# Performance work log

Hardware: AMD Instinct MI355X
Metric: run time of the kernel (lower is better)

The kernel has to match this reference:

```python
import jax, jax.numpy as jnp
import numpy as np


def _dct_basis(N):
    # X[k] = 2 * sum_n x[n] * cos(pi * k * (2n+1) / (2N))  -- matches the
    # flip+concat+rfft+twiddle path of the torch module (unnormalized DCT-II x2).
    k = jnp.arange(N, dtype=jnp.float32)[:, None]
    n = jnp.arange(N, dtype=jnp.float32)[None, :]
    return 2.0 * jnp.cos(jnp.pi * k * (2.0 * n + 1.0) / (2.0 * N))  # (K, N)


def _dct2(x):
    B, C, H, W = x.shape
    Bw = _dct_basis(W)
    Bh = _dct_basis(H)
    x = jnp.einsum('bchw,kw->bchk', x, Bw)  # DCT along W
    x = jnp.einsum('bchw,kh->bckw', x, Bh)  # DCT along H
    return x


def _conv3x3(x, w, b):
    y = jax.lax.conv_general_dilated(x, w, window_strides=(1, 1), padding='SAME',
                                     dimension_numbers=('NCHW', 'OIHW', 'NCHW'))
    return y + b[None, :, None, None]


def _bn(x, g, be, m, v):
    # inference-mode BatchNorm2d, eps = 1e-5
    inv = jax.lax.rsqrt(v + 1e-5)
    return (x - m[None, :, None, None]) * (g * inv)[None, :, None, None] + be[None, :, None, None]


def setup_inputs() -> dict:
    key = jax.random.key(0)
    ks = jax.random.split(key, 16)
    B, C, H, W = 32, 1, 224, 224
    mid, emb = 128, 256
    s = 0.05
    return {
        'x':  jax.random.normal(ks[0], (B, C, H, W), jnp.float32),
        'w1': jax.random.normal(ks[1], (64, C, 3, 3), jnp.float32) * s,
        'b1': jax.random.normal(ks[2], (64,), jnp.float32) * s,
        'g1': jax.random.uniform(ks[3], (64,), jnp.float32, 0.5, 1.5),
        'be1': jax.random.normal(ks[4], (64,), jnp.float32) * s,
        'm1': jax.random.normal(ks[5], (64,), jnp.float32) * s,
        'v1': jax.random.uniform(ks[6], (64,), jnp.float32, 0.5, 1.5),
        'w2': jax.random.normal(ks[7], (mid, 64, 3, 3), jnp.float32) * s,
        'b2': jax.random.normal(ks[8], (mid,), jnp.float32) * s,
        'g2': jax.random.uniform(ks[9], (mid,), jnp.float32, 0.5, 1.5),
        'be2': jax.random.normal(ks[10], (mid,), jnp.float32) * s,
        'm2': jax.random.normal(ks[11], (mid,), jnp.float32) * s,
        'v2': jax.random.uniform(ks[12], (mid,), jnp.float32, 0.5, 1.5),
        'wp': jax.random.normal(ks[13], (emb, mid), jnp.float32) * s,
        'bp': jax.random.normal(ks[14], (emb,), jnp.float32) * s,
    }


def reference(x, w1, b1, g1, be1, m1, v1, w2, b2, g2, be2, m2, v2, wp, bp):
    USE_TOPK = 0.5
    X = _dct2(x)                                   # (B, 1, H, W)
    B, C, H, W = X.shape
    k_h, k_w = int(H * USE_TOPK), int(W * USE_TOPK)
    mask = jnp.zeros((H, W), X.dtype).at[:k_h, :k_w].set(1.0)
    X = X * mask[None, None]
    h = jax.nn.relu(_bn(_conv3x3(X, w1, b1), g1, be1, m1, v1))
    h = jax.nn.relu(_bn(_conv3x3(h, w2, b2), g2, be2, m2, v2))
    h = jnp.mean(h, axis=(2, 3))                   # AdaptiveAvgPool2d((1,1)) -> (B, mid)
    return h @ wp.T + bp                           # (B, emb_dim)
```

## Files before the change

kernel.cpp:

```cpp
#include <hip/hip_runtime.h>
#include <math.h>


#define NPIX 224
#define KEEP 112
#define H1DIM 115
#define NPX1 (H1DIM * H1DIM)
#define ADIM 114

typedef short bf16x8 __attribute__((ext_vector_type(8)));
typedef float f32x4  __attribute__((ext_vector_type(4)));
typedef float f32x16 __attribute__((ext_vector_type(16)));

__device__ __forceinline__ unsigned short f2bf(float f) {
    unsigned int u = __float_as_uint(f);
    unsigned int r = (u + 0x7FFFu + ((u >> 16) & 1u)) >> 16;
    return (unsigned short)r;
}

__global__ __launch_bounds__(256) void prep_kernel(
    const float* __restrict__ w1, const float* __restrict__ b1,
    const float* __restrict__ g1, const float* __restrict__ be1,
    const float* __restrict__ m1, const float* __restrict__ v1,
    const float* __restrict__ w2,
    float* __restrict__ Bst, float* __restrict__ P,
    float* __restrict__ ws1, float* __restrict__ wb1,
    uint4* __restrict__ w2f) {
    int bx = blockIdx.x, tid = threadIdx.x;
    if (bx < 49) {
        int idx = bx * 256 + tid;
        if (idx < KEEP * KEEP) {
            int n = idx / KEEP, k = idx - n * KEEP;
            double ang = 3.14159265358979323846 * (double)k * (2.0 * n + 1.0) / (2.0 * NPIX);
            Bst[n * KEEP + k] = (float)(2.0 * cos(ang));
        }
    } else if (bx < 54) {
        __shared__ float c1s[64];
        if (tid < 64) {
            float sc = g1[tid] * rsqrtf(v1[tid] + 1e-5f);
            c1s[tid] = fmaxf((b1[tid] - m1[tid]) * sc + be1[tid], 0.f);
        }
        __syncthreads();
        int idx = (bx - 49) * 256 + tid;
        if (idx < 128 * 9) {
            int oc = idx / 9, tap = idx - oc * 9;
            float s = 0.f;
            for (int ic = 0; ic < 64; ++ic)
                s = fmaf(w2[((size_t)oc * 64 + ic) * 9 + tap], c1s[ic], s);
            P[idx] = s;
        }
    } else if (bx == 54) {
        if (tid < 64) {
            float sc = g1[tid] * rsqrtf(v1[tid] + 1e-5f);
            wb1[tid] = (b1[tid] - m1[tid]) * sc + be1[tid];
            for (int t = 0; t < 9; ++t) ws1[tid * 9 + t] = w1[tid * 9 + t] * sc;
        }
    } else {
        int j = (bx - 55) * 256 + tid;
        if (j < 9216) {
            int q = j >> 6, lane = j & 63;
            int tap = q / 16, rem = q & 15;
            int kc = rem >> 2, g32 = rem & 3;
            int oc = g32 * 32 + (lane & 31);
            int ic0 = kc * 16 + (lane >> 5) * 8;
            union { unsigned short us[8]; uint4 v; } u;
#pragma unroll
            for (int t_ = 0; t_ < 8; ++t_)
                u.us[t_] = f2bf(w2[((size_t)oc * 64 + ic0 + t_) * 9 + tap]);
            w2f[j] = u.v;
        }
    }
}

__global__ __launch_bounds__(128) void dct_w_kernel(const float* __restrict__ x,
                                                    const float* __restrict__ Bst,
                                                    float* __restrict__ tmp1) {
    int blk = blockIdx.x;
    int tid = threadIdx.x;
    __shared__ float eo[2][4][112];
    const float* rows = x + (size_t)blk * 4 * NPIX;
    for (int i = tid; i < 448; i += 128) {
        int r = i / 112, n = i - r * 112;
        float a = rows[r * NPIX + n], bv = rows[r * NPIX + 223 - n];
        eo[0][r][n] = a + bv;
        eo[1][r][n] = a - bv;
    }
    __syncthreads();
    int kw = tid;
    if (kw >= KEEP) return;
    const float* eop = &eo[kw & 1][0][0];
    float a0 = 0.f, a1 = 0.f, a2 = 0.f, a3 = 0.f;
    for (int n = 0; n < 112; ++n) {
        float bs = Bst[n * KEEP + kw];
        a0 = fmaf(eop[n], bs, a0);
        a1 = fmaf(eop[112 + n], bs, a1);
        a2 = fmaf(eop[224 + n], bs, a2);
        a3 = fmaf(eop[336 + n], bs, a3);
    }
    size_t base = (size_t)blk * 4 * KEEP + kw;
    tmp1[base] = a0; tmp1[base + 112] = a1; tmp1[base + 224] = a2; tmp1[base + 336] = a3;
}

__global__ __launch_bounds__(512) void dct_h_kernel(const float* __restrict__ tmp1,
                                                    const float* __restrict__ Bst,
                                                    float* __restrict__ Xd) {
    int kq = blockIdx.x, b = blockIdx.y;
    int tid = threadIdx.x;
    int kw = tid & 127, sub = tid >> 7;
    __shared__ float ps[3][4][112];
    const int kh0 = kq * 4;
    float a0 = 0.f, a1 = 0.f, a2 = 0.f, a3 = 0.f;
    if (kw < KEEP) {
        const float* t = tmp1 + (size_t)b * NPIX * KEEP + kw;
        for (int h = sub * 28; h < sub * 28 + 28; ++h) {
            float lo = t[(size_t)h * KEEP];
            float hi = t[(size_t)(223 - h) * KEEP];
            float e = lo + hi, o = lo - hi;
            const float* bs = Bst + h * KEEP + kh0;
            a0 = fmaf(e, bs[0], a0);
            a1 = fmaf(o, bs[1], a1);
            a2 = fmaf(e, bs[2], a2);
            a3 = fmaf(o, bs[3], a3);
        }
        if (sub) {
            ps[sub - 1][0][kw] = a0; ps[sub - 1][1][kw] = a1;
            ps[sub - 1][2][kw] = a2; ps[sub - 1][3][kw] = a3;
        }
    }
    __syncthreads();
    if (sub == 0 && kw < KEEP) {
        a0 += ps[0][0][kw] + ps[1][0][kw] + ps[2][0][kw];
        a1 += ps[0][1][kw] + ps[1][1][kw] + ps[2][1][kw];
        a2 += ps[0][2][kw] + ps[1][2][kw] + ps[2][2][kw];
        a3 += ps[0][3][kw] + ps[1][3][kw] + ps[2][3][kw];
        float* X = Xd + ((size_t)b * KEEP + kh0) * KEEP + kw;
        X[0] = a0; X[112] = a1; X[224] = a2; X[336] = a3;
    }
}

__global__ __launch_bounds__(256) void conv1_kernel(const float* __restrict__ Xd,
                                                    const float* __restrict__ ws1,
                                                    const float* __restrict__ wb1,
                                                    unsigned short* __restrict__ h1c) {
    const int b = blockIdx.y;
    const int p0 = blockIdx.x * 256;
    const int tid = threadIdx.x;
    const int p = p0 + tid;
    __shared__ uint4 Lt[2048];

    const bool valid = p < NPX1;
    int r = p / H1DIM, c = p - r * H1DIM;
    const float* X = Xd + (size_t)b * KEEP * KEEP;
    float xv[9];
#pragma unroll
    for (int ky = 0; ky < 3; ++ky)
#pragma unroll
        for (int kx = 0; kx < 3; ++kx) {
            int rr = r + ky - 1, cc = c + kx - 1;
            xv[ky * 3 + kx] =
                (valid && (unsigned)rr < (unsigned)KEEP && (unsigned)cc < (unsigned)KEEP)
                    ? X[rr * KEEP + cc] : 0.f;
        }

#pragma unroll 1
    for (int icg = 0; icg < 8; ++icg) {
        union { unsigned short us[8]; uint4 v; } u;
#pragma unroll
        for (int j = 0; j < 8; ++j) {
            int ic = icg * 8 + j;
            float s = wb1[ic];
#pragma unroll
            for (int t = 0; t < 9; ++t) s = fmaf(xv[t], ws1[ic * 9 + t], s);
            u.us[j] = f2bf(fmaxf(s, 0.f));
        }
        Lt[tid * 8 + (icg ^ (tid & 7))] = u.v;
    }
    __syncthreads();

#pragma unroll
    for (int k = 0; k < 8; ++k) {
        int q = k * 256 + tid;
        int pxl = q >> 3, ig = q & 7;
        uint4 v = Lt[pxl * 8 + (ig ^ (pxl & 7))];
        int pg = p0 + pxl;
        if (pg < NPX1)
            *reinterpret_cast<uint4*>(h1c + ((size_t)b * NPX1 + pg) * 64 + ig * 8) = v;
    }
}

__global__ __launch_bounds__(512, 4) void conv2_mfma_kernel(
    const unsigned short* __restrict__ h1c, const uint4* __restrict__ w2f,
    const float* __restrict__ b2, const float* __restrict__ g2,
    const float* __restrict__ be2, const float* __restrict__ m2,
    const float* __restrict__ v2, float* __restrict__ partial) {
    const int tc = blockIdx.x, tr = blockIdx.y, b = blockIdx.z;
    const int r0 = tr * 16, c0 = tc * 16;
    const int tid = threadIdx.x;
    const int lane = tid & 63, w = tid >> 6;
    const int mg = w & 3, og = w >> 2;

    __shared__ unsigned short At[324 * 64];

    const unsigned short* __restrict__ h1b = h1c + (size_t)b * (NPX1 * 64);
    char* Atw = reinterpret_cast<char*>(At);
    for (int e = tid; e < 2592; e += 512) {
        int px = e >> 3, gi = e & 7;
        int pr = px / 18, pc = px - pr * 18;
        int gr = r0 + pr - 1, gc = c0 + pc - 1;
        uint4 v = make_uint4(0u, 0u, 0u, 0u);
        if ((unsigned)gr < (unsigned)H1DIM && (unsigned)gc < (unsigned)H1DIM)
            v = *reinterpret_cast<const uint4*>(h1b + ((size_t)(gr * H1DIM + gc)) * 64 + gi * 8);
        int off = px * 128 + 32 * ((gi >> 1) ^ (px & 3)) + 16 * ((gi & 1) ^ ((px >> 2) & 1));
        *reinterpret_cast<uint4*>(Atw + off) = v;
    }
    __syncthreads();

    f32x16 acc[2][2];
#pragma unroll
    for (int F = 0; F < 2; ++F)
#pragma unroll
        for (int N = 0; N < 2; ++N)
#pragma unroll
            for (int i = 0; i < 16; ++i) acc[F][N][i] = 0.f;

    const int flim2 = ADIM - r0 - 4 * mg;
    int A0[9];
    {
        const int prb = 4 * mg + ((lane & 31) >> 4);
        const int cb = lane & 15;
        const int hb = lane >> 5;
#pragma unroll
        for (int ky = 0; ky < 3; ++ky)
#pragma unroll
            for (int kx = 0; kx < 3; ++kx) {
                int px = (prb + ky) * 18 + cb + kx;
                A0[ky * 3 + kx] = px * 128 + 32 * (px & 3) + 16 * (hb ^ ((px >> 2) & 1));
            }
    }
    const char* Atc = reinterpret_cast<const char*>(At);

    if (flim2 >= 4) {
#pragma unroll
        for (int s = 0; s < 36; ++s) {
            const int tap = s >> 2, kc = s & 3;
            const int ky = tap / 3, kx = tap - 3 * ky;
            const bf16x8* bq = reinterpret_cast<const bf16x8*>(
                w2f + (size_t)(((tap * 4 + kc) * 4) + og * 2) * 64 + lane);
            const bf16x8 b0 = bq[0];
            const bf16x8 b1 = bq[64];
            const int a0 = A0[ky * 3 + kx] ^ (kc << 5);
            const int a1 = (a0 ^ 16) + 4608;
            const bf16x8 va0 = *reinterpret_cast<const bf16x8*>(Atc + a0);
            const bf16x8 va1 = *reinterpret_cast<const bf16x8*>(Atc + a1);
            acc[0][0] = __builtin_amdgcn_mfma_f32_32x32x16_bf16(va0, b0, acc[0][0], 0, 0, 0);
            acc[0][1] = __builtin_amdgcn_mfma_f32_32x32x16_bf16(va0, b1, acc[0][1], 0, 0, 0);
            acc[1][0] = __builtin_amdgcn_mfma_f32_32x32x16_bf16(va1, b0, acc[1][0], 0, 0, 0);
            acc[1][1] = __builtin_amdgcn_mfma_f32_32x32x16_bf16(va1, b1, acc[1][1], 0, 0, 0);
        }
    } else if (flim2 > 0) {
#pragma unroll
        for (int s = 0; s < 36; ++s) {
            const int tap = s >> 2, kc = s & 3;
            const int ky = tap / 3, kx = tap - 3 * ky;
            const bf16x8* bq = reinterpret_cast<const bf16x8*>(
                w2f + (size_t)(((tap * 4 + kc) * 4) + og * 2) * 64 + lane);
            const bf16x8 b0 = bq[0];
            const bf16x8 b1 = bq[64];
            const int a0 = A0[ky * 3 + kx] ^ (kc << 5);
            const bf16x8 va0 = *reinterpret_cast<const bf16x8*>(Atc + a0);
            acc[0][0] = __builtin_amdgcn_mfma_f32_32x32x16_bf16(va0, b0, acc[0][0], 0, 0, 0);
            acc[0][1] = __builtin_amdgcn_mfma_f32_32x32x16_bf16(va0, b1, acc[0][1], 0, 0, 0);
        }
    }

    const int tile = tr * 8 + tc;
    float* pslice = partial + (((size_t)b * 64 + tile) * 4 + mg) * 128;
#pragma unroll
    for (int N = 0; N < 2; ++N) {
        int oc = og * 64 + N * 32 + (lane & 31);
        float sc = g2[oc] * rsqrtf(v2[oc] + 1e-5f);
        float bias = b2[oc] - m2[oc];
        float add = be2[oc];
        float s = 0.f;
#pragma unroll
        for (int F = 0; F < 2; ++F) {
#pragma unroll
            for (int rg = 0; rg < 16; ++rg) {
                int m = (rg & 3) + 8 * (rg >> 2) + 4 * (lane >> 5);
                int p = ((2 * mg + F) << 5) + m;
                int row = r0 + (p >> 4);
                int col = c0 + (p & 15);
                float v = fmaxf(fmaf(acc[F][N][rg] + bias, sc, add), 0.f);
                s += (row < ADIM && col < ADIM) ? v : 0.f;
            }
        }
        s += __shfl_xor(s, 32);
        if (lane < 32) pslice[og * 64 + N * 32 + lane] = s;
    }
}

__global__ __launch_bounds__(256) void reduce_mean_kernel(
    const float* __restrict__ partial, const float* __restrict__ P,
    const float* __restrict__ b2, const float* __restrict__ g2,
    const float* __restrict__ be2, const float* __restrict__ m2,
    const float* __restrict__ v2, float* __restrict__ mean) {
    int b = blockIdx.x, ocg = blockIdx.y;
    int tid = threadIdx.x;
    int ocl = tid & 15, jq = tid >> 4;
    int oc = ocg * 16 + ocl;
    const float* pb = partial + (size_t)b * 256 * 128 + oc;
    float s = 0.f;
#pragma unroll
    for (int jj = 0; jj < 16; ++jj) s += pb[(size_t)(jq * 16 + jj) * 128];
    __shared__ float red[16][17];
    red[jq][ocl] = s;
    __syncthreads();
    if (jq == 0) {
        float tot = 0.f;
#pragma unroll
        for (int k = 0; k < 16; ++k) tot += red[k][ocl];

        float p[9];
#pragma unroll
        for (int t = 0; t < 9; ++t) p[t] = P[oc * 9 + t];

        float Sall = p[0] + p[1] + p[2] + p[3] + p[4] + p[5] + p[6] + p[7] + p[8];
        float Stop = p[3] + p[4] + p[5] + p[6] + p[7] + p[8];
        float Sbot = p[0] + p[1] + p[2] + p[3] + p[4] + p[5];
        float Sleft  = p[1] + p[2] + p[4] + p[5] + p[7] + p[8];
        float Sright = p[0] + p[1] + p[3] + p[4] + p[6] + p[7];
        float Ctr = p[3] + p[4] + p[6] + p[7];
        float Cbl = p[1] + p[2] + p[4] + p[5];
        float Cbr = p[0] + p[1] + p[3] + p[4];

        float bias = b2[oc], mm = m2[oc], bb = be2[oc];
        float sc = g2[oc] * rsqrtf(v2[oc] + 1e-5f);
#define VALOF(S) fmaxf(((bias) + (S) - (mm)) * (sc) + (bb), 0.f)
        float cs = 36515.f * VALOF(Sall) + 109.f * VALOF(Stop) + 109.f * VALOF(Sleft)
                 + 222.f * VALOF(Sbot) + 222.f * VALOF(Sright)
                 + VALOF(Ctr) + VALOF(Cbl) + VALOF(Cbr);
#undef VALOF
        mean[b * 128 + oc] = (tot + cs) * (1.f / (224.f * 224.f));
    }
}

__global__ __launch_bounds__(256) void final_linear_kernel(const float* __restrict__ mean,
                                                           const float* __restrict__ wp,
                                                           const float* __restrict__ bp,
                                                           float* __restrict__ out) {
    int b = blockIdx.x, e = threadIdx.x;
    __shared__ float mrow[128];
    if (threadIdx.x < 128) mrow[threadIdx.x] = mean[b * 128 + threadIdx.x];
    __syncthreads();
    const float4* wr = reinterpret_cast<const float4*>(wp + (size_t)e * 128);
    float s = bp[e];
#pragma unroll 8
    for (int c = 0; c < 32; ++c) {
        float4 wv = wr[c];
        s = fmaf(mrow[4 * c], wv.x, s);
        s = fmaf(mrow[4 * c + 1], wv.y, s);
        s = fmaf(mrow[4 * c + 2], wv.z, s);
        s = fmaf(mrow[4 * c + 3], wv.w, s);
    }
    out[(size_t)b * 256 + e] = s;
}

extern "C" void kernel_launch(void* const* d_in, const int* in_sizes, int n_in,
                              void* d_out, int out_size, void* d_ws, size_t ws_size,
                              hipStream_t stream) {
    const float* x   = (const float*)d_in[0];
    const float* w1  = (const float*)d_in[1];
    const float* b1  = (const float*)d_in[2];
    const float* g1  = (const float*)d_in[3];
    const float* be1 = (const float*)d_in[4];
    const float* m1  = (const float*)d_in[5];
    const float* v1  = (const float*)d_in[6];
    const float* w2  = (const float*)d_in[7];
    const float* b2  = (const float*)d_in[8];
    const float* g2  = (const float*)d_in[9];
    const float* be2 = (const float*)d_in[10];
    const float* m2  = (const float*)d_in[11];
    const float* v2  = (const float*)d_in[12];
    const float* wp  = (const float*)d_in[13];
    const float* bp  = (const float*)d_in[14];
    float* out = (float*)d_out;

    float* ws = (float*)d_ws;
    size_t off = 0;
    float* Bst  = ws + off; off += (size_t)KEEP * KEEP;
    float* tmp1 = ws + off; off += (size_t)32 * NPIX * KEEP;
    float* Xd   = ws + off; off += (size_t)32 * KEEP * KEEP;
    float* P    = ws + off; off += 128 * 9;
    float* ws1  = ws + off; off += 64 * 9;
    float* wb1  = ws + off; off += 64;
    uint4* w2f  = (uint4*)(ws + off); off += (size_t)9216 * 4;
    float* part = ws + off; off += (size_t)32 * 256 * 128;
    float* mean = ws + off; off += 32 * 128;
    unsigned short* h1c = (unsigned short*)(ws + off);
    off += (size_t)32 * NPX1 * 64 / 2;

    if (ws_size < off * sizeof(float)) return;

    prep_kernel<<<dim3(91), dim3(256), 0, stream>>>(w1, b1, g1, be1, m1, v1, w2,
                                                    Bst, P, ws1, wb1, w2f);
    dct_w_kernel<<<dim3(32 * 56), dim3(128), 0, stream>>>(x, Bst, tmp1);
    dct_h_kernel<<<dim3(28, 32), dim3(512), 0, stream>>>(tmp1, Bst, Xd);
    conv1_kernel<<<dim3(52, 32), dim3(256), 0, stream>>>(Xd, ws1, wb1, h1c);
    conv2_mfma_kernel<<<dim3(8, 8, 32), dim3(512), 0, stream>>>(
        h1c, w2f, b2, g2, be2, m2, v2, part);
    reduce_mean_kernel<<<dim3(32, 8), dim3(256), 0, stream>>>(part, P, b2, g2, be2, m2, v2, mean);
    final_linear_kernel<<<dim3(32), dim3(256), 0, stream>>>(mean, wp, bp, out);
}
```

Measured before the change: 125.1 us.

## Enlarge conv2 tiles with split-channel staging, fuse reduce and linear tail

The conv2 MFMA kernel now covers 32x16 output tiles per block, with four row fragments per wave. It stages the input halo in two 32-channel halves through a smaller shared buffer, so each weight fragment feeds more MFMAs and far fewer blocks are launched. The reduce-mean and final linear kernels are merged into one tail kernel, and the DCT-W kernel now handles 8 rows per block with 256 threads. The cost is more accumulator registers (occupancy hint lowered to 2), an extra barrier per channel half, and per-fragment predicates in the inner loop.

```diff
diff --git a/kernel.cpp b/kernel.cpp
--- a/kernel.cpp
+++ b/kernel.cpp
@@ -9,7 +9,6 @@
 #define ADIM 114
 
 typedef short bf16x8 __attribute__((ext_vector_type(8)));
-typedef float f32x4  __attribute__((ext_vector_type(4)));
 typedef float f32x16 __attribute__((ext_vector_type(16)));
 
 __device__ __forceinline__ unsigned short f2bf(float f) {
@@ -26,22 +25,22 @@
     float* __restrict__ Bst, float* __restrict__ P,
     float* __restrict__ ws1, float* __restrict__ wb1,
     uint4* __restrict__ w2f) {
-    int bx = blockIdx.x, tid = threadIdx.x;
-    if (bx < 49) {
-        int idx = bx * 256 + tid;
+    int bp = blockIdx.x, tid = threadIdx.x;
+    if (bp < 49) {
+        int idx = bp * 256 + tid;
         if (idx < KEEP * KEEP) {
             int n = idx / KEEP, k = idx - n * KEEP;
             double ang = 3.14159265358979323846 * (double)k * (2.0 * n + 1.0) / (2.0 * NPIX);
             Bst[n * KEEP + k] = (float)(2.0 * cos(ang));
         }
-    } else if (bx < 54) {
+    } else if (bp < 54) {
         __shared__ float c1s[64];
         if (tid < 64) {
             float sc = g1[tid] * rsqrtf(v1[tid] + 1e-5f);
             c1s[tid] = fmaxf((b1[tid] - m1[tid]) * sc + be1[tid], 0.f);
         }
         __syncthreads();
-        int idx = (bx - 49) * 256 + tid;
+        int idx = (bp - 49) * 256 + tid;
         if (idx < 128 * 9) {
             int oc = idx / 9, tap = idx - oc * 9;
             float s = 0.f;
@@ -49,20 +48,20 @@
                 s = fmaf(w2[((size_t)oc * 64 + ic) * 9 + tap], c1s[ic], s);
             P[idx] = s;
         }
-    } else if (bx == 54) {
+    } else if (bp == 54) {
         if (tid < 64) {
             float sc = g1[tid] * rsqrtf(v1[tid] + 1e-5f);
             wb1[tid] = (b1[tid] - m1[tid]) * sc + be1[tid];
             for (int t = 0; t < 9; ++t) ws1[tid * 9 + t] = w1[tid * 9 + t] * sc;
         }
     } else {
-        int j = (bx - 55) * 256 + tid;
+        int j = (bp - 55) * 256 + tid;
         if (j < 9216) {
             int q = j >> 6, lane = j & 63;
             int tap = q / 16, rem = q & 15;
-            int kc = rem >> 2, g32 = rem & 3;
+            int kcq = rem >> 2, g32 = rem & 3;
             int oc = g32 * 32 + (lane & 31);
-            int ic0 = kc * 16 + (lane >> 5) * 8;
+            int ic0 = kcq * 16 + (lane >> 5) * 8;
             union { unsigned short us[8]; uint4 v; } u;
 #pragma unroll
             for (int t_ = 0; t_ < 8; ++t_)
@@ -72,23 +71,22 @@
     }
 }
 
-__global__ __launch_bounds__(128) void dct_w_kernel(const float* __restrict__ x,
+__global__ __launch_bounds__(256) void dct_w_kernel(const float* __restrict__ x,
                                                     const float* __restrict__ Bst,
                                                     float* __restrict__ tmp1) {
-    int blk = blockIdx.x;
-    int tid = threadIdx.x;
-    __shared__ float eo[2][4][112];
-    const float* rows = x + (size_t)blk * 4 * NPIX;
-    for (int i = tid; i < 448; i += 128) {
+    int bx = blockIdx.x, tid = threadIdx.x;
+    __shared__ float eo[2][8][112];
+    const float* rows = x + (size_t)bx * 8 * NPIX;
+    for (int i = tid; i < 896; i += 256) {
         int r = i / 112, n = i - r * 112;
         float a = rows[r * NPIX + n], bv = rows[r * NPIX + 223 - n];
         eo[0][r][n] = a + bv;
         eo[1][r][n] = a - bv;
     }
     __syncthreads();
-    int kw = tid;
+    int kw = tid & 127, rh = tid >> 7;
     if (kw >= KEEP) return;
-    const float* eop = &eo[kw & 1][0][0];
+    const float* eop = &eo[kw & 1][rh * 4][0];
     float a0 = 0.f, a1 = 0.f, a2 = 0.f, a3 = 0.f;
     for (int n = 0; n < 112; ++n) {
         float bs = Bst[n * KEEP + kw];
@@ -97,7 +95,7 @@
         a2 = fmaf(eop[224 + n], bs, a2);
         a3 = fmaf(eop[336 + n], bs, a3);
     }
-    size_t base = (size_t)blk * 4 * KEEP + kw;
+    size_t base = ((size_t)bx * 8 + rh * 4) * KEEP + kw;
     tmp1[base] = a0; tmp1[base + 112] = a1; tmp1[base + 224] = a2; tmp1[base + 336] = a3;
 }
 
@@ -188,142 +186,143 @@
     }
 }
 
-__global__ __launch_bounds__(512, 4) void conv2_mfma_kernel(
+__global__ __launch_bounds__(512, 2) void conv2_mfma_kernel(
     const unsigned short* __restrict__ h1c, const uint4* __restrict__ w2f,
     const float* __restrict__ b2, const float* __restrict__ g2,
     const float* __restrict__ be2, const float* __restrict__ m2,
     const float* __restrict__ v2, float* __restrict__ partial) {
     const int tc = blockIdx.x, tr = blockIdx.y, b = blockIdx.z;
-    const int r0 = tr * 16, c0 = tc * 16;
+    const int r0 = tr * 32, c0 = tc * 16;
     const int tid = threadIdx.x;
     const int lane = tid & 63, w = tid >> 6;
-    const int mg = w & 3, og = w >> 2;
-
-    __shared__ unsigned short At[324 * 64];
-
-    const unsigned short* __restrict__ h1b = h1c + (size_t)b * (NPX1 * 64);
-    char* Atw = reinterpret_cast<char*>(At);
-    for (int e = tid; e < 2592; e += 512) {
-        int px = e >> 3, gi = e & 7;
-        int pr = px / 18, pc = px - pr * 18;
-        int gr = r0 + pr - 1, gc = c0 + pc - 1;
-        uint4 v = make_uint4(0u, 0u, 0u, 0u);
-        if ((unsigned)gr < (unsigned)H1DIM && (unsigned)gc < (unsigned)H1DIM)
-            v = *reinterpret_cast<const uint4*>(h1b + ((size_t)(gr * H1DIM + gc)) * 64 + gi * 8);
-        int off = px * 128 + 32 * ((gi >> 1) ^ (px & 3)) + 16 * ((gi & 1) ^ ((px >> 2) & 1));
-        *reinterpret_cast<uint4*>(Atw + off) = v;
-    }
-    __syncthreads();
-
-    f32x16 acc[2][2];
-#pragma unroll
-    for (int F = 0; F < 2; ++F)
+    const int mgr = w & 3, ogr = w >> 2;
+
+    __shared__ uint4 AtV[2448];
+    char* Atw = reinterpret_cast<char*>(AtV);
+    const char* Atc = reinterpret_cast<const char*>(AtV);
+
+    f32x16 acc[4][2];
+#pragma unroll
+    for (int F = 0; F < 4; ++F)
 #pragma unroll
         for (int N = 0; N < 2; ++N)
 #pragma unroll
             for (int i = 0; i < 16; ++i) acc[F][N][i] = 0.f;
 
-    const int flim2 = ADIM - r0 - 4 * mg;
     int A0[9];
     {
-        const int prb = 4 * mg + ((lane & 31) >> 4);
+        const int rb = 2 * mgr + ((lane & 31) >> 4);
         const int cb = lane & 15;
         const int hb = lane >> 5;
 #pragma unroll
         for (int ky = 0; ky < 3; ++ky)
 #pragma unroll
             for (int kx = 0; kx < 3; ++kx) {
-                int px = (prb + ky) * 18 + cb + kx;
-                A0[ky * 3 + kx] = px * 128 + 32 * (px & 3) + 16 * (hb ^ ((px >> 2) & 1));
+                int px = (rb + ky) * 18 + cb + kx;
+                int pairp = px >> 1;
+                int s = ((px & 1) << 2) | hb;
+                A0[ky * 3 + kx] = pairp * 128 + 16 * (s ^ (pairp & 7));
             }
     }
-    const char* Atc = reinterpret_cast<const char*>(At);
-
-    if (flim2 >= 4) {
-#pragma unroll
-        for (int s = 0; s < 36; ++s) {
-            const int tap = s >> 2, kc = s & 3;
-            const int ky = tap / 3, kx = tap - 3 * ky;
-            const bf16x8* bq = reinterpret_cast<const bf16x8*>(
-                w2f + (size_t)(((tap * 4 + kc) * 4) + og * 2) * 64 + lane);
-            const bf16x8 b0 = bq[0];
-            const bf16x8 b1 = bq[64];
-            const int a0 = A0[ky * 3 + kx] ^ (kc << 5);
-            const int a1 = (a0 ^ 16) + 4608;
-            const bf16x8 va0 = *reinterpret_cast<const bf16x8*>(Atc + a0);
-            const bf16x8 va1 = *reinterpret_cast<const bf16x8*>(Atc + a1);
-            acc[0][0] = __builtin_amdgcn_mfma_f32_32x32x16_bf16(va0, b0, acc[0][0], 0, 0, 0);
-            acc[0][1] = __builtin_amdgcn_mfma_f32_32x32x16_bf16(va0, b1, acc[0][1], 0, 0, 0);
-            acc[1][0] = __builtin_amdgcn_mfma_f32_32x32x16_bf16(va1, b0, acc[1][0], 0, 0, 0);
-            acc[1][1] = __builtin_amdgcn_mfma_f32_32x32x16_bf16(va1, b1, acc[1][1], 0, 0, 0);
-        }
-    } else if (flim2 > 0) {
-#pragma unroll
-        for (int s = 0; s < 36; ++s) {
-            const int tap = s >> 2, kc = s & 3;
-            const int ky = tap / 3, kx = tap - 3 * ky;
-            const bf16x8* bq = reinterpret_cast<const bf16x8*>(
-                w2f + (size_t)(((tap * 4 + kc) * 4) + og * 2) * 64 + lane);
-            const bf16x8 b0 = bq[0];
-            const bf16x8 b1 = bq[64];
-            const int a0 = A0[ky * 3 + kx] ^ (kc << 5);
-            const bf16x8 va0 = *reinterpret_cast<const bf16x8*>(Atc + a0);
-            acc[0][0] = __builtin_amdgcn_mfma_f32_32x32x16_bf16(va0, b0, acc[0][0], 0, 0, 0);
-            acc[0][1] = __builtin_amdgcn_mfma_f32_32x32x16_bf16(va0, b1, acc[0][1], 0, 0, 0);
+    const int wrow0 = r0 + 2 * mgr;
+    const bool d1 = wrow0 + 8 < ADIM, d2 = wrow0 + 16 < ADIM, d3 = wrow0 + 24 < ADIM;
+
+    const unsigned short* __restrict__ h1b = h1c + (size_t)b * (NPX1 * 64);
+
+#pragma unroll 1
+    for (int icq = 0; icq < 2; ++icq) {
+        if (icq) __syncthreads();
+        for (int e = tid; e < 2448; e += 512) {
+            int pxp = e >> 3, g = e & 7;
+            int px = 2 * pxp + (g >> 2);
+            int pr = px / 18, pc = px - pr * 18;
+            int gr = r0 + pr - 1, gc = c0 + pc - 1;
+            uint4 v = make_uint4(0u, 0u, 0u, 0u);
+            if ((unsigned)gr < (unsigned)H1DIM && (unsigned)gc < (unsigned)H1DIM)
+                v = *reinterpret_cast<const uint4*>(
+                    h1b + ((size_t)(gr * H1DIM + gc)) * 64 + icq * 32 + (g & 3) * 8);
+            *reinterpret_cast<uint4*>(Atw + pxp * 128 + 16 * (g ^ (pxp & 7))) = v;
+        }
+        __syncthreads();
+
+#pragma unroll
+        for (int kc = 0; kc < 2; ++kc) {
+#pragma unroll
+            for (int tap = 0; tap < 9; ++tap) {
+                const uint4* bq =
+                    w2f + (size_t)(((tap * 4 + icq * 2 + kc) * 4) + ogr * 2) * 64 + lane;
+                const bf16x8 B0 = *reinterpret_cast<const bf16x8*>(bq);
+                const bf16x8 B1 = *reinterpret_cast<const bf16x8*>(bq + 64);
+                const int ad = A0[tap] ^ (kc << 5);
+                const bf16x8 a0 = *reinterpret_cast<const bf16x8*>(Atc + ad);
+                acc[0][0] = __builtin_amdgcn_mfma_f32_32x32x16_bf16(a0, B0, acc[0][0], 0, 0, 0);
+                acc[0][1] = __builtin_amdgcn_mfma_f32_32x32x16_bf16(a0, B1, acc[0][1], 0, 0, 0);
+                if (d1) {
+                    const bf16x8 a1 = *reinterpret_cast<const bf16x8*>(Atc + ad + 9216);
+                    acc[1][0] = __builtin_amdgcn_mfma_f32_32x32x16_bf16(a1, B0, acc[1][0], 0, 0, 0);
+                    acc[1][1] = __builtin_amdgcn_mfma_f32_32x32x16_bf16(a1, B1, acc[1][1], 0, 0, 0);
+                }
+                if (d2) {
+                    const bf16x8 a2 = *reinterpret_cast<const bf16x8*>(Atc + ad + 18432);
+                    acc[2][0] = __builtin_amdgcn_mfma_f32_32x32x16_bf16(a2, B0, acc[2][0], 0, 0, 0);
+                    acc[2][1] = __builtin_amdgcn_mfma_f32_32x32x16_bf16(a2, B1, acc[2][1], 0, 0, 0);
+                }
+                if (d3) {
+                    const bf16x8 a3 = *reinterpret_cast<const bf16x8*>(Atc + ad + 27648);
+                    acc[3][0] = __builtin_amdgcn_mfma_f32_32x32x16_bf16(a3, B0, acc[3][0], 0, 0, 0);
+                    acc[3][1] = __builtin_amdgcn_mfma_f32_32x32x16_bf16(a3, B1, acc[3][1], 0, 0, 0);
+                }
+            }
         }
     }
 
     const int tile = tr * 8 + tc;
-    float* pslice = partial + (((size_t)b * 64 + tile) * 4 + mg) * 128;
+    float* prow = partial + (((size_t)b * 32 + tile) * 4 + mgr) * 128;
 #pragma unroll
     for (int N = 0; N < 2; ++N) {
-        int oc = og * 64 + N * 32 + (lane & 31);
+        int oc = ogr * 64 + N * 32 + (lane & 31);
         float sc = g2[oc] * rsqrtf(v2[oc] + 1e-5f);
         float bias = b2[oc] - m2[oc];
         float add = be2[oc];
         float s = 0.f;
 #pragma unroll
-        for (int F = 0; F < 2; ++F) {
+        for (int F = 0; F < 4; ++F) {
 #pragma unroll
             for (int rg = 0; rg < 16; ++rg) {
                 int m = (rg & 3) + 8 * (rg >> 2) + 4 * (lane >> 5);
-                int p = ((2 * mg + F) << 5) + m;
-                int row = r0 + (p >> 4);
-                int col = c0 + (p & 15);
+                int row = wrow0 + 8 * F + (m >> 4);
+                int col = c0 + (m & 15);
                 float v = fmaxf(fmaf(acc[F][N][rg] + bias, sc, add), 0.f);
                 s += (row < ADIM && col < ADIM) ? v : 0.f;
             }
         }
         s += __shfl_xor(s, 32);
-        if (lane < 32) pslice[og * 64 + N * 32 + lane] = s;
-    }
-}
-
-__global__ __launch_bounds__(256) void reduce_mean_kernel(
+        if (lane < 32) prow[ogr * 64 + N * 32 + lane] = s;
+    }
+}
+
+__global__ __launch_bounds__(256) void tail_kernel(
     const float* __restrict__ partial, const float* __restrict__ P,
     const float* __restrict__ b2, const float* __restrict__ g2,
     const float* __restrict__ be2, const float* __restrict__ m2,
-    const float* __restrict__ v2, float* __restrict__ mean) {
-    int b = blockIdx.x, ocg = blockIdx.y;
-    int tid = threadIdx.x;
-    int ocl = tid & 15, jq = tid >> 4;
-    int oc = ocg * 16 + ocl;
-    const float* pb = partial + (size_t)b * 256 * 128 + oc;
+    const float* __restrict__ v2,
+    const float* __restrict__ wp, const float* __restrict__ bp,
+    float* __restrict__ out) {
+    int b = blockIdx.x, tid = threadIdx.x;
+    __shared__ float red[2][128];
+    __shared__ float mrow[128];
+    int oc = tid & 127, half = tid >> 7;
+    const float* pb = partial + (size_t)b * 128 * 128 + oc;
     float s = 0.f;
-#pragma unroll
-    for (int jj = 0; jj < 16; ++jj) s += pb[(size_t)(jq * 16 + jj) * 128];
-    __shared__ float red[16][17];
-    red[jq][ocl] = s;
+#pragma unroll 8
+    for (int j = 0; j < 64; ++j) s += pb[(size_t)(half * 64 + j) * 128];
+    red[half][oc] = s;
     __syncthreads();
-    if (jq == 0) {
-        float tot = 0.f;
-#pragma unroll
-        for (int k = 0; k < 16; ++k) tot += red[k][ocl];
-
+    if (tid < 128) {
+        float tot = red[0][tid] + red[1][tid];
         float p[9];
 #pragma unroll
-        for (int t = 0; t < 9; ++t) p[t] = P[oc * 9 + t];
-
+        for (int t = 0; t < 9; ++t) p[t] = P[tid * 9 + t];
         float Sall = p[0] + p[1] + p[2] + p[3] + p[4] + p[5] + p[6] + p[7] + p[8];
         float Stop = p[3] + p[4] + p[5] + p[6] + p[7] + p[8];
         float Sbot = p[0] + p[1] + p[2] + p[3] + p[4] + p[5];
@@ -332,37 +331,27 @@
         float Ctr = p[3] + p[4] + p[6] + p[7];
         float Cbl = p[1] + p[2] + p[4] + p[5];
         float Cbr = p[0] + p[1] + p[3] + p[4];
-
-        float bias = b2[oc], mm = m2[oc], bb = be2[oc];
-        float sc = g2[oc] * rsqrtf(v2[oc] + 1e-5f);
+        float bias = b2[tid], mm = m2[tid], bb = be2[tid];
+        float sc = g2[tid] * rsqrtf(v2[tid] + 1e-5f);
 #define VALOF(S) fmaxf(((bias) + (S) - (mm)) * (sc) + (bb), 0.f)
         float cs = 36515.f * VALOF(Sall) + 109.f * VALOF(Stop) + 109.f * VALOF(Sleft)
                  + 222.f * VALOF(Sbot) + 222.f * VALOF(Sright)
                  + VALOF(Ctr) + VALOF(Cbl) + VALOF(Cbr);
 #undef VALOF
-        mean[b * 128 + oc] = (tot + cs) * (1.f / (224.f * 224.f));
-    }
-}
-
-__global__ __launch_bounds__(256) void final_linear_kernel(const float* __restrict__ mean,
-                                                           const float* __restrict__ wp,
-                                                           const float* __restrict__ bp,
-                                                           float* __restrict__ out) {
-    int b = blockIdx.x, e = threadIdx.x;
-    __shared__ float mrow[128];
-    if (threadIdx.x < 128) mrow[threadIdx.x] = mean[b * 128 + threadIdx.x];
+        mrow[tid] = (tot + cs) * (1.f / (224.f * 224.f));
+    }
     __syncthreads();
-    const float4* wr = reinterpret_cast<const float4*>(wp + (size_t)e * 128);
-    float s = bp[e];
+    const float4* wr = reinterpret_cast<const float4*>(wp + (size_t)tid * 128);
+    float acc = bp[tid];
 #pragma unroll 8
     for (int c = 0; c < 32; ++c) {
         float4 wv = wr[c];
-        s = fmaf(mrow[4 * c], wv.x, s);
-        s = fmaf(mrow[4 * c + 1], wv.y, s);
-        s = fmaf(mrow[4 * c + 2], wv.z, s);
-        s = fmaf(mrow[4 * c + 3], wv.w, s);
-    }
-    out[(size_t)b * 256 + e] = s;
+        acc = fmaf(mrow[4 * c], wv.x, acc);
+        acc = fmaf(mrow[4 * c + 1], wv.y, acc);
+        acc = fmaf(mrow[4 * c + 2], wv.z, acc);
+        acc = fmaf(mrow[4 * c + 3], wv.w, acc);
+    }
+    out[(size_t)b * 256 + tid] = acc;
 }
 
 extern "C" void kernel_launch(void* const* d_in, const int* in_sizes, int n_in,
@@ -394,8 +383,7 @@
     float* ws1  = ws + off; off += 64 * 9;
     float* wb1  = ws + off; off += 64;
     uint4* w2f  = (uint4*)(ws + off); off += (size_t)9216 * 4;
-    float* part = ws + off; off += (size_t)32 * 256 * 128;
-    float* mean = ws + off; off += 32 * 128;
+    float* part = ws + off; off += (size_t)32 * 128 * 128;
     unsigned short* h1c = (unsigned short*)(ws + off);
     off += (size_t)32 * NPX1 * 64 / 2;
 
@@ -403,11 +391,10 @@
 
     prep_kernel<<<dim3(91), dim3(256), 0, stream>>>(w1, b1, g1, be1, m1, v1, w2,
                                                     Bst, P, ws1, wb1, w2f);
-    dct_w_kernel<<<dim3(32 * 56), dim3(128), 0, stream>>>(x, Bst, tmp1);
+    dct_w_kernel<<<dim3(896), dim3(256), 0, stream>>>(x, Bst, tmp1);
     dct_h_kernel<<<dim3(28, 32), dim3(512), 0, stream>>>(tmp1, Bst, Xd);
     conv1_kernel<<<dim3(52, 32), dim3(256), 0, stream>>>(Xd, ws1, wb1, h1c);
-    conv2_mfma_kernel<<<dim3(8, 8, 32), dim3(512), 0, stream>>>(
+    conv2_mfma_kernel<<<dim3(8, 4, 32), dim3(512), 0, stream>>>(
         h1c, w2f, b2, g2, be2, m2, v2, part);
-    reduce_mean_kernel<<<dim3(32, 8), dim3(256), 0, stream>>>(part, P, b2, g2, be2, m2, v2, mean);
-    final_linear_kernel<<<dim3(32), dim3(256), 0, stream>>>(mean, wp, bp, out);
-}
+    tail_kernel<<<dim3(32), dim3(256), 0, stream>>>(part, P, b2, g2, be2, m2, v2, wp, bp, out);
+}
```

Result: slower. 136.2 us (+8.9%).
